# Kernel tuning notes

Hardware: AMD Instinct MI355X
Metric: run time of the kernel (lower is better)

## Reference

```python
import jax, jax.numpy as jnp
import numpy as np

N_NODES = 100000
N_EDGES = 1600000
IN_CH = 64
OUT_CH = 64


def setup_inputs() -> dict:
    key = jax.random.key(0)
    k1, k2, k3, k4, k5, k6 = jax.random.split(key, 6)
    x = jax.random.normal(k1, (N_NODES, IN_CH), dtype=jnp.float32)
    edge_index = jax.random.randint(k2, (2, N_EDGES), 0, N_NODES, dtype=jnp.int64)
    edge_attr = jax.random.uniform(k3, (N_EDGES, 3), dtype=jnp.float32)
    root_weight = jax.random.normal(k4, (IN_CH, OUT_CH), dtype=jnp.float32)
    bias = jax.random.normal(k5, (OUT_CH,), dtype=jnp.float32)
    gaussian_param = jnp.ones((1,), dtype=jnp.float32)
    return {"x": x, "edge_index": edge_index, "edge_attr": edge_attr,
            "root_weight": root_weight, "bias": bias,
            "gaussian_param": gaussian_param}


def reference(x, edge_index, edge_attr, root_weight, bias, gaussian_param):
    src = edge_index[0]
    tgt = edge_index[1]
    # per-edge gaussian weight from distance (edge_attr[:, 0])
    dist = edge_attr[:, 0:1]                                  # [E, 1]
    gw = jnp.exp(-dist ** 2 / (gaussian_param ** 2 + 1e-8))   # [E, 1]
    # gather -> matmul -> scale
    messages = (x[src] @ root_weight) * gw                    # [E, out]
    # scatter-add to target nodes
    out = jax.ops.segment_sum(messages, tgt, num_segments=x.shape[0])
    out = out + x @ root_weight + bias
    return out
```

## Files before the change

kernel.cpp:

```cpp
#include <hip/hip_runtime.h>
#include <hip/hip_bf16.h>
#include <stdint.h>

#define N_NODES 100000
#define N_EDGES 1600000
#define CH 64

#define NPB 128
#define NBUCK ((N_NODES + NPB - 1) / NPB)
#define CHUNK 4096
#define BT 1024
#define EPT (CHUNK / BT)
#define NBLK_E ((N_EDGES + CHUNK - 1) / CHUNK)

#define STRIDE 2560
#define CAP 3072
#define ST 512

#define GM 64

typedef float f32x4 __attribute__((ext_vector_type(4)));

__device__ __forceinline__ unsigned short bf16rn(float f) {
  unsigned u = __float_as_uint(f);
  unsigned r = u + 0x7FFFu + ((u >> 16) & 1u);
  return (unsigned short)(r >> 16);
}


__global__ __launch_bounds__(BT) void bin2_kernel(const int* __restrict__ ei,
                                                  const float* __restrict__ attr,
                                                  const float* __restrict__ gp,
                                                  int* __restrict__ gcur,
                                                  uint2* __restrict__ recs,
                                                  const float* __restrict__ x,
                                                  unsigned short* __restrict__ xh) {
  __shared__ int lhist[NBUCK];
  __shared__ int lbase[NBUCK];
  const int tid = threadIdx.x;
  for (int i = tid; i < NBUCK; i += BT) lhist[i] = 0;
  __syncthreads();
  const int cbase = blockIdx.x * CHUNK;
  const float inv = 1.0f / (gp[0] * gp[0] + 1e-8f);

  int s[EPT], t[EPT], lrank[EPT];
  float g[EPT];
#pragma unroll
  for (int k = 0; k < EPT; ++k) {
    const int e = cbase + k * BT + tid;
    if (e < N_EDGES) {
      s[k] = ei[e];
      t[k] = ei[N_EDGES + e];
      const float d = attr[3 * e];
      g[k] = __expf(-d * d * inv);
      lrank[k] = atomicAdd(&lhist[t[k] >> 7], 1);
    }
  }
  {
    const int nq = N_NODES * CH / 4;
    const int stride = gridDim.x * BT;
    for (int q = blockIdx.x * BT + tid; q < nq; q += stride) {
      const float4 v = reinterpret_cast<const float4*>(x)[q];
      ushort4 o;
      o.x = bf16rn(v.x);
      o.y = bf16rn(v.y);
      o.z = bf16rn(v.z);
      o.w = bf16rn(v.w);
      reinterpret_cast<ushort4*>(xh)[q] = o;
    }
  }
  __syncthreads();
  for (int i = tid; i < NBUCK; i += BT) {
    const int c = lhist[i];
    if (c) lbase[i] = i * STRIDE + atomicAdd(&gcur[i], c);
  }
  __syncthreads();

#pragma unroll
  for (int k = 0; k < EPT; ++k) {
    const int e = cbase + k * BT + tid;
    if (e < N_EDGES) {
      const int bb = t[k] >> 7;
      const int idx = lbase[bb] + lrank[k];
      if (idx < (bb + 1) * STRIDE) {
        uint2 rec;
        rec.x = (unsigned)s[k] | ((unsigned)(t[k] & (NPB - 1)) << 17);
        rec.y = __float_as_uint(g[k]);
        recs[idx] = rec;
      }
    }
  }
}

__global__ __launch_bounds__(ST) void sortb2_kernel(const int* __restrict__ gcur,
                                                    uint2* __restrict__ recs,
                                                    int* __restrict__ offs,
                                                    int* __restrict__ ends) {
  __shared__ uint2 srec[STRIDE];
  __shared__ int lhist[NPB];
  __shared__ int lofs[NPB];
  __shared__ int lcur[NPB];
  const int b = blockIdx.x;
  const int tid = threadIdx.x;
  const int start = b * STRIDE;
  int cnt = gcur[b];
  cnt = cnt < STRIDE ? cnt : STRIDE;

  if (tid < NPB) lhist[tid] = 0;
  __syncthreads();
  for (int i = tid; i < cnt; i += ST) {
    const uint2 r = recs[start + i];
    srec[i] = r;
    atomicAdd(&lhist[r.x >> 17], 1);
  }
  __syncthreads();
  if (tid < NPB) lofs[tid] = lhist[tid];
  __syncthreads();
  for (int off = 1; off < NPB; off <<= 1) {
    int t = 0;
    if (tid < NPB && tid >= off) t = lofs[tid - off];
    __syncthreads();
    if (tid < NPB) lofs[tid] += t;
    __syncthreads();
  }
  if (tid < NPB) {
    const int incl = lofs[tid];
    const int excl = incl - lhist[tid];
    lcur[tid] = excl;
    const int node = b * NPB + tid;
    if (node < N_NODES) {
      offs[node] = start + excl;
      ends[node] = start + incl;
    }
  }
  __syncthreads();
  for (int i = tid; i < cnt; i += ST) {
    const uint2 r = srec[i];
    const int pos = atomicAdd(&lcur[r.x >> 17], 1);
    recs[start + pos] = r;
  }
}


__global__ __launch_bounds__(BT) void hist2_kernel(const int* __restrict__ ei,
                                                   int* __restrict__ ghist,
                                                   const float* __restrict__ x,
                                                   unsigned short* __restrict__ xh,
                                                   int do_conv) {
  __shared__ int lh[NBUCK];
  const int tid = threadIdx.x;
  for (int i = tid; i < NBUCK; i += BT) lh[i] = 0;
  __syncthreads();
  const int cbase = blockIdx.x * CHUNK;
#pragma unroll
  for (int k = 0; k < EPT; ++k) {
    const int e = cbase + k * BT + tid;
    if (e < N_EDGES) atomicAdd(&lh[ei[N_EDGES + e] >> 7], 1);
  }
  if (do_conv) {
    const int nq = N_NODES * CH / 4;
    const int stride = gridDim.x * BT;
    for (int q = blockIdx.x * BT + tid; q < nq; q += stride) {
      const float4 v = reinterpret_cast<const float4*>(x)[q];
      ushort4 o;
      o.x = bf16rn(v.x);
      o.y = bf16rn(v.y);
      o.z = bf16rn(v.z);
      o.w = bf16rn(v.w);
      reinterpret_cast<ushort4*>(xh)[q] = o;
    }
  }
  __syncthreads();
  for (int i = tid; i < NBUCK; i += BT) {
    const int c = lh[i];
    if (c) atomicAdd(&ghist[i], c);
  }
}

__global__ __launch_bounds__(1024) void scan_kernel(const int* __restrict__ ghist,
                                                    int* __restrict__ gbase,
                                                    int* __restrict__ gcur) {
  __shared__ int sd[1024];
  const int tid = threadIdx.x;
  const int v = (tid < NBUCK) ? ghist[tid] : 0;
  sd[tid] = v;
  __syncthreads();
  for (int off = 1; off < 1024; off <<= 1) {
    int t = (tid >= off) ? sd[tid - off] : 0;
    __syncthreads();
    sd[tid] += t;
    __syncthreads();
  }
  if (tid < NBUCK) {
    const int excl = sd[tid] - v;
    gbase[tid] = excl;
    gcur[tid] = excl;
  }
}

__global__ __launch_bounds__(BT) void bin_kernel(const int* __restrict__ ei,
                                                 const float* __restrict__ attr,
                                                 const float* __restrict__ gp,
                                                 int* __restrict__ gcur,
                                                 uint2* __restrict__ recs) {
  __shared__ int lhist[NBUCK];
  __shared__ int lbase[NBUCK];
  const int tid = threadIdx.x;
  for (int i = tid; i < NBUCK; i += BT) lhist[i] = 0;
  __syncthreads();
  const int cbase = blockIdx.x * CHUNK;
  const float inv = 1.0f / (gp[0] * gp[0] + 1e-8f);

  int s[EPT], t[EPT], lrank[EPT];
  float g[EPT];
#pragma unroll
  for (int k = 0; k < EPT; ++k) {
    const int e = cbase + k * BT + tid;
    if (e < N_EDGES) {
      s[k] = ei[e];
      t[k] = ei[N_EDGES + e];
      const float d = attr[3 * e];
      g[k] = __expf(-d * d * inv);
      lrank[k] = atomicAdd(&lhist[t[k] >> 7], 1);
    }
  }
  __syncthreads();
  for (int i = tid; i < NBUCK; i += BT) {
    const int c = lhist[i];
    if (c) lbase[i] = atomicAdd(&gcur[i], c);
  }
  __syncthreads();

#pragma unroll
  for (int k = 0; k < EPT; ++k) {
    const int e = cbase + k * BT + tid;
    if (e < N_EDGES) {
      uint2 rec;
      rec.x = (unsigned)s[k] | ((unsigned)(t[k] & (NPB - 1)) << 17);
      rec.y = __float_as_uint(g[k]);
      recs[lbase[t[k] >> 7] + lrank[k]] = rec;
    }
  }
}

__global__ __launch_bounds__(ST) void sortb_kernel(const int* __restrict__ gbase,
                                                   const int* __restrict__ ghist,
                                                   uint2* __restrict__ recs,
                                                   int* __restrict__ offs) {
  __shared__ uint2 srec[CAP];
  __shared__ int lhist[NPB];
  __shared__ int lofs[NPB];
  __shared__ int lcur[NPB];
  const int b = blockIdx.x;
  const int tid = threadIdx.x;
  const int start = gbase[b];
  const int cnt = ghist[b] < CAP ? ghist[b] : CAP;

  if (tid < NPB) lhist[tid] = 0;
  __syncthreads();
  for (int i = tid; i < cnt; i += ST) {
    const uint2 r = recs[start + i];
    srec[i] = r;
    atomicAdd(&lhist[r.x >> 17], 1);
  }
  __syncthreads();
  if (tid < NPB) lofs[tid] = lhist[tid];
  __syncthreads();
  for (int off = 1; off < NPB; off <<= 1) {
    int t = 0;
    if (tid < NPB && tid >= off) t = lofs[tid - off];
    __syncthreads();
    if (tid < NPB) lofs[tid] += t;
    __syncthreads();
  }
  if (tid < NPB) {
    const int excl = lofs[tid] - lhist[tid];
    lcur[tid] = excl;
    const int node = b * NPB + tid;
    if (node < N_NODES) offs[node] = start + excl;
  }
  if (b == NBUCK - 1 && tid == 0) offs[N_NODES] = start + cnt;
  __syncthreads();
  for (int i = tid; i < cnt; i += ST) {
    const uint2 r = srec[i];
    const int pos = atomicAdd(&lcur[r.x >> 17], 1);
    recs[start + pos] = r;
  }
}


__global__ __launch_bounds__(256) void reduce7h_kernel(
    const unsigned short* __restrict__ xh, const int* __restrict__ offs,
    const int* __restrict__ ends, const uint2* __restrict__ recs,
    float* __restrict__ out) {
  const int node = (blockIdx.x * blockDim.x + threadIdx.x) >> 6;
  if (node >= N_NODES) return;
  const int lane = threadIdx.x & 63;
  const int c2 = lane & 31;
  const int eh = lane >> 5;
  const int n0 = __builtin_amdgcn_readfirstlane(offs[node]);
  const int n1 = __builtin_amdgcn_readfirstlane(ends[node]);
  const int m = n1 - n0;

  float ax = 0.0f, ay = 0.0f;
  int j = 0;
  for (; j + 16 <= m; j += 16) {
#pragma unroll
    for (int p = 0; p < 8; ++p) {
      const uint2 r0 = recs[n0 + j + 2 * p];
      const uint2 r1 = recs[n0 + j + 2 * p + 1];
      const unsigned sx = (eh ? r1.x : r0.x) & 0x1FFFFu;
      const float g = __uint_as_float(eh ? r1.y : r0.y);
      const unsigned u =
          *reinterpret_cast<const unsigned*>(&xh[(size_t)sx * CH + c2 * 2]);
      ax += g * __uint_as_float(u << 16);
      ay += g * __uint_as_float(u & 0xFFFF0000u);
    }
  }
  for (; j + 8 <= m; j += 8) {
#pragma unroll
    for (int p = 0; p < 4; ++p) {
      const uint2 r0 = recs[n0 + j + 2 * p];
      const uint2 r1 = recs[n0 + j + 2 * p + 1];
      const unsigned sx = (eh ? r1.x : r0.x) & 0x1FFFFu;
      const float g = __uint_as_float(eh ? r1.y : r0.y);
      const unsigned u =
          *reinterpret_cast<const unsigned*>(&xh[(size_t)sx * CH + c2 * 2]);
      ax += g * __uint_as_float(u << 16);
      ay += g * __uint_as_float(u & 0xFFFF0000u);
    }
  }
  for (; j < m; j += 2) {
    const uint2 r0 = recs[n0 + j];
    uint2 r1 = {0u, 0u};
    if (j + 1 < m) r1 = recs[n0 + j + 1];
    const unsigned sx = (eh ? r1.x : r0.x) & 0x1FFFFu;
    const float g = __uint_as_float(eh ? r1.y : r0.y);
    const unsigned u =
        *reinterpret_cast<const unsigned*>(&xh[(size_t)sx * CH + c2 * 2]);
    ax += g * __uint_as_float(u << 16);
    ay += g * __uint_as_float(u & 0xFFFF0000u);
  }
  ax += __shfl_xor(ax, 32);
  ay += __shfl_xor(ay, 32);
  if (lane < 32) {
    float2 o;
    o.x = ax;
    o.y = ay;
    reinterpret_cast<float2*>(out + (size_t)node * CH)[c2] = o;
  }
}

__global__ __launch_bounds__(256) void reduce3_kernel(
    const float* __restrict__ x, const int* __restrict__ offs,
    const uint2* __restrict__ recs, float* __restrict__ out) {
  const int node = (blockIdx.x * blockDim.x + threadIdx.x) >> 6;
  if (node >= N_NODES) return;
  const int lane = threadIdx.x & 63;
  const int n0 = offs[node];
  const int m = offs[node + 1] - n0;

  float acc = 0.0f;
  for (int base = 0; base < m; base += 64) {
    const int mm = (m - base) < 64 ? (m - base) : 64;
    uint2 pr = {0u, 0u};
    if (lane < mm) pr = recs[n0 + base + lane];
    const int pk_all = (int)pr.x;
    const float g_all = __uint_as_float(pr.y);
    int j = 0;
    for (; j + 4 <= mm; j += 4) {
      const int s0 = __shfl(pk_all, j + 0) & 0x1FFFF;
      const int s1 = __shfl(pk_all, j + 1) & 0x1FFFF;
      const int s2 = __shfl(pk_all, j + 2) & 0x1FFFF;
      const int s3 = __shfl(pk_all, j + 3) & 0x1FFFF;
      const float g0 = __shfl(g_all, j + 0);
      const float g1 = __shfl(g_all, j + 1);
      const float g2 = __shfl(g_all, j + 2);
      const float g3 = __shfl(g_all, j + 3);
      acc += g0 * x[(size_t)s0 * CH + lane] + g1 * x[(size_t)s1 * CH + lane] +
             g2 * x[(size_t)s2 * CH + lane] + g3 * x[(size_t)s3 * CH + lane];
    }
    for (; j < mm; ++j) {
      const int sj = __shfl(pk_all, j) & 0x1FFFF;
      const float gj = __shfl(g_all, j);
      acc += gj * x[(size_t)sj * CH + lane];
    }
  }
  out[(size_t)node * CH + lane] = acc + x[(size_t)node * CH + lane];
}

__global__ __launch_bounds__(256) void scatter_kernel(
    const float* __restrict__ x, const int* __restrict__ ei,
    const float* __restrict__ attr, const float* __restrict__ gp,
    float* __restrict__ agg) {
  const int lane = threadIdx.x & 63;
  const int wave = (blockIdx.x * blockDim.x + threadIdx.x) >> 6;
  const int nwaves = (gridDim.x * blockDim.x) >> 6;
  const float inv = 1.0f / (gp[0] * gp[0] + 1e-8f);
  for (int base = wave * 64; base < N_EDGES; base += nwaves * 64) {
    const int e = base + lane;
    const int s = ei[e];
    const int t = ei[N_EDGES + e];
    const float d = attr[3 * e];
    const float g = __expf(-d * d * inv);
#pragma unroll 1
    for (int j = 0; j < 64; ++j) {
      const int sj = __shfl(s, j);
      const int tj = __shfl(t, j);
      const float gj = __shfl(g, j);
      atomicAdd(&agg[(size_t)tj * CH + lane], gj * x[sj * CH + lane]);
    }
  }
}

__global__ __launch_bounds__(256) void rowgemm4_kernel(
    const float* __restrict__ x, const float* __restrict__ W,
    const float* __restrict__ bias, float* __restrict__ out) {
  __shared__ float sT[64][GM + 4];
  __shared__ float wl[64 * 64];
  const int tid = threadIdx.x;
  const int node0 = blockIdx.x * GM;

  {
    const float4* W4 = reinterpret_cast<const float4*>(W);
    float4* wl4 = reinterpret_cast<float4*>(wl);
#pragma unroll
    for (int i = 0; i < 4; ++i) wl4[i * 256 + tid] = W4[i * 256 + tid];
  }
  {
    const int m = tid >> 2;
    const int kq = tid & 3;
    if (node0 + m < N_NODES) {
      const float4* r4 =
          reinterpret_cast<const float4*>(out + (size_t)(node0 + m) * CH);
      const float4* x4 =
          reinterpret_cast<const float4*>(x + (size_t)(node0 + m) * CH);
#pragma unroll
      for (int q = 0; q < 4; ++q) {
        const float4 v = r4[kq * 4 + q];
        const float4 xv = x4[kq * 4 + q];
        const int k = kq * 16 + q * 4;
        sT[k + 0][m] = v.x + xv.x;
        sT[k + 1][m] = v.y + xv.y;
        sT[k + 2][m] = v.z + xv.z;
        sT[k + 3][m] = v.w + xv.w;
      }
    }
  }
  __syncthreads();

  const int m0 = (tid >> 4) * 4;
  const int c0 = (tid & 15) * 4;

  const f32x4 b4 = *reinterpret_cast<const f32x4*>(&bias[c0]);
  f32x4 acc0 = b4, acc1 = b4, acc2 = b4, acc3 = b4;

#pragma unroll 8
  for (int k = 0; k < 64; ++k) {
    const f32x4 sv = *reinterpret_cast<const f32x4*>(&sT[k][m0]);
    const f32x4 wv = *reinterpret_cast<const f32x4*>(&wl[k * 64 + c0]);
    acc0 += sv.x * wv;
    acc1 += sv.y * wv;
    acc2 += sv.z * wv;
    acc3 += sv.w * wv;
  }

  __syncthreads();
  f32x4 accs[4] = {acc0, acc1, acc2, acc3};
#pragma unroll
  for (int i = 0; i < 4; ++i) {
    const int node = node0 + m0 + i;
    if (node < N_NODES)
      *reinterpret_cast<f32x4*>(&out[(size_t)node * CH + c0]) = accs[i];
  }
}

__global__ __launch_bounds__(256) void rowgemm3_kernel(
    const float* __restrict__ W, const float* __restrict__ bias,
    float* __restrict__ out) {
  __shared__ float sT[64][GM + 4];
  __shared__ float wl[64 * 64];
  const int tid = threadIdx.x;
  const int node0 = blockIdx.x * GM;

  {
    const float4* W4 = reinterpret_cast<const float4*>(W);
    float4* wl4 = reinterpret_cast<float4*>(wl);
#pragma unroll
    for (int i = 0; i < 4; ++i) wl4[i * 256 + tid] = W4[i * 256 + tid];
  }
  {
    const int m = tid >> 2;
    const int kq = tid & 3;
    if (node0 + m < N_NODES) {
      const float4* r4 =
          reinterpret_cast<const float4*>(out + (size_t)(node0 + m) * CH);
#pragma unroll
      for (int q = 0; q < 4; ++q) {
        const float4 v = r4[kq * 4 + q];
        const int k = kq * 16 + q * 4;
        sT[k + 0][m] = v.x;
        sT[k + 1][m] = v.y;
        sT[k + 2][m] = v.z;
        sT[k + 3][m] = v.w;
      }
    }
  }
  __syncthreads();

  const int m0 = (tid >> 4) * 4;
  const int c0 = (tid & 15) * 4;

  const f32x4 b4 = *reinterpret_cast<const f32x4*>(&bias[c0]);
  f32x4 acc0 = b4, acc1 = b4, acc2 = b4, acc3 = b4;

#pragma unroll 8
  for (int k = 0; k < 64; ++k) {
    const f32x4 sv = *reinterpret_cast<const f32x4*>(&sT[k][m0]);
    const f32x4 wv = *reinterpret_cast<const f32x4*>(&wl[k * 64 + c0]);
    acc0 += sv.x * wv;
    acc1 += sv.y * wv;
    acc2 += sv.z * wv;
    acc3 += sv.w * wv;
  }

  __syncthreads();
  f32x4 accs[4] = {acc0, acc1, acc2, acc3};
#pragma unroll
  for (int i = 0; i < 4; ++i) {
    const int node = node0 + m0 + i;
    if (node < N_NODES)
      *reinterpret_cast<f32x4*>(&out[(size_t)node * CH + c0]) = accs[i];
  }
}

__global__ __launch_bounds__(256) void rowgemm_kernel(
    const float* __restrict__ x, const float* __restrict__ W,
    const float* __restrict__ bias, float* __restrict__ out) {
  const int r = blockIdx.x * blockDim.x + threadIdx.x;
  if (r >= N_NODES) return;
  const float* xr = x + (size_t)r * CH;
  float* outr = out + (size_t)r * CH;

  float s[CH];
#pragma unroll
  for (int k4 = 0; k4 < CH / 4; ++k4) {
    float4 xv = *reinterpret_cast<const float4*>(xr + k4 * 4);
    float4 av = *reinterpret_cast<const float4*>(outr + k4 * 4);
    s[k4 * 4 + 0] = xv.x + av.x;
    s[k4 * 4 + 1] = xv.y + av.y;
    s[k4 * 4 + 2] = xv.z + av.z;
    s[k4 * 4 + 3] = xv.w + av.w;
  }

  float acc[CH];
#pragma unroll
  for (int c = 0; c < CH; ++c) acc[c] = bias[c];

#pragma unroll
  for (int k = 0; k < CH; ++k) {
    const float sk = s[k];
#pragma unroll
    for (int c4 = 0; c4 < CH / 4; ++c4) {
      const float4 w = *reinterpret_cast<const float4*>(&W[k * CH + c4 * 4]);
      acc[c4 * 4 + 0] += sk * w.x;
      acc[c4 * 4 + 1] += sk * w.y;
      acc[c4 * 4 + 2] += sk * w.z;
      acc[c4 * 4 + 3] += sk * w.w;
    }
  }

#pragma unroll
  for (int c4 = 0; c4 < CH / 4; ++c4) {
    float4 o = {acc[c4 * 4 + 0], acc[c4 * 4 + 1], acc[c4 * 4 + 2],
                acc[c4 * 4 + 3]};
    *reinterpret_cast<float4*>(outr + c4 * 4) = o;
  }
}

extern "C" void kernel_launch(void* const* d_in, const int* in_sizes, int n_in,
                              void* d_out, int out_size, void* d_ws,
                              size_t ws_size, hipStream_t stream) {
  const float* x = (const float*)d_in[0];
  const int* ei = (const int*)d_in[1];
  const float* attr = (const float*)d_in[2];
  const float* W = (const float*)d_in[3];
  const float* bias = (const float*)d_in[4];
  const float* gp = (const float*)d_in[5];
  float* out = (float*)d_out;

  const size_t sz_i = ((size_t)NBUCK * 4 + 255) & ~(size_t)255;
  const size_t sz_xh = (size_t)N_NODES * CH * 2;
  const size_t sz_offs1 = ((size_t)N_NODES * 4 + 255) & ~(size_t)255;

  const size_t sz_recsA = (size_t)NBUCK * STRIDE * 8;
  const size_t need_fs = sz_i + sz_recsA + 2 * sz_offs1 + sz_xh;

  const size_t sz_recsB = (size_t)N_EDGES * 8;
  const size_t sz_offsB = ((size_t)(N_NODES + 1) * 4 + 255) & ~(size_t)255;
  const size_t need_b = 3 * sz_i + sz_recsB + sz_offsB;
  const size_t need_a = need_b + sz_xh;

  if (ws_size >= need_fs) {
    char* base = (char*)d_ws;
    int* gcur = (int*)base;
    uint2* recs = (uint2*)(base + sz_i);
    int* offs = (int*)(base + sz_i + sz_recsA);
    int* ends = (int*)(base + sz_i + sz_recsA + sz_offs1);
    unsigned short* xh =
        (unsigned short*)(base + sz_i + sz_recsA + 2 * sz_offs1);

    hipMemsetAsync(gcur, 0, (size_t)NBUCK * 4, stream);
    bin2_kernel<<<NBLK_E, BT, 0, stream>>>(ei, attr, gp, gcur, recs, x, xh);
    sortb2_kernel<<<NBUCK, ST, 0, stream>>>(gcur, recs, offs, ends);
    reduce7h_kernel<<<(N_NODES * 64 + 255) / 256, 256, 0, stream>>>(
        xh, offs, ends, recs, out);
    rowgemm4_kernel<<<(N_NODES + GM - 1) / GM, 256, 0, stream>>>(x, W, bias,
                                                                 out);
  } else if (ws_size >= need_b) {
    char* base = (char*)d_ws;
    int* ghist = (int*)base;
    int* gbase = (int*)(base + sz_i);
    int* gcur = (int*)(base + 2 * sz_i);
    uint2* recs = (uint2*)(base + 3 * sz_i);
    int* offs = (int*)(base + 3 * sz_i + sz_recsB);
    unsigned short* xh = (unsigned short*)(base + need_b);

    const int tier_a = (ws_size >= need_a) ? 1 : 0;
    hipMemsetAsync(ghist, 0, (size_t)NBUCK * 4, stream);
    hist2_kernel<<<NBLK_E, BT, 0, stream>>>(ei, ghist, x, xh, tier_a);
    scan_kernel<<<1, 1024, 0, stream>>>(ghist, gbase, gcur);
    bin_kernel<<<NBLK_E, BT, 0, stream>>>(ei, attr, gp, gcur, recs);
    sortb_kernel<<<NBUCK, ST, 0, stream>>>(gbase, ghist, recs, offs);
    if (tier_a) {
      reduce7h_kernel<<<(N_NODES * 64 + 255) / 256, 256, 0, stream>>>(
          xh, offs, offs + 1, recs, out);
      rowgemm4_kernel<<<(N_NODES + GM - 1) / GM, 256, 0, stream>>>(x, W, bias,
                                                                   out);
    } else {
      reduce3_kernel<<<(N_NODES * 64 + 255) / 256, 256, 0, stream>>>(x, offs,
                                                                     recs, out);
      rowgemm3_kernel<<<(N_NODES + GM - 1) / GM, 256, 0, stream>>>(W, bias,
                                                                   out);
    }
  } else {
    hipMemsetAsync(out, 0, (size_t)N_NODES * CH * sizeof(float), stream);
    scatter_kernel<<<2048, 256, 0, stream>>>(x, ei, attr, gp, out);
    rowgemm_kernel<<<(N_NODES + 255) / 256, 256, 0, stream>>>(x, W, bias, out);
  }
}
```

Measured before the change: 105.7 us.

## Store edge aggregate as bf16 scratch and fuse add into row GEMM

A new reduce kernel writes the per-node gathered-x aggregate as packed bf16 to a workspace buffer instead of fp32 into the output. A new row-GEMM kernel reads that aggregate, adds x, and does a single matmul with bias, so the output is written once rather than written and then read back. The sort kernel's block size also grows from 512 to 1024 threads. This cuts HBM traffic for the aggregate, but rounding the sum to bf16 adds precision loss and the path needs extra workspace.

```diff
diff --git a/kernel.cpp b/kernel.cpp
--- a/kernel.cpp
+++ b/kernel.cpp
@@ -15,7 +15,7 @@
 
 #define STRIDE 2560
 #define CAP 3072
-#define ST 512
+#define ST 1024
 
 #define GM 64
 
@@ -25,6 +25,10 @@
   unsigned u = __float_as_uint(f);
   unsigned r = u + 0x7FFFu + ((u >> 16) & 1u);
   return (unsigned short)(r >> 16);
+}
+
+__device__ __forceinline__ float bf16f(unsigned short h) {
+  return __uint_as_float((unsigned)h << 16);
 }
 
 
@@ -288,6 +292,67 @@
   }
 }
 
+
+__global__ __launch_bounds__(256) void reduce7hb_kernel(
+    const unsigned short* __restrict__ xh, const int* __restrict__ offs,
+    const int* __restrict__ ends, const uint2* __restrict__ recs,
+    unsigned* __restrict__ aggh) {
+  const int node = (blockIdx.x * blockDim.x + threadIdx.x) >> 6;
+  if (node >= N_NODES) return;
+  const int lane = threadIdx.x & 63;
+  const int c2 = lane & 31;
+  const int eh = lane >> 5;
+  const int n0 = __builtin_amdgcn_readfirstlane(offs[node]);
+  const int n1 = __builtin_amdgcn_readfirstlane(ends[node]);
+  const int m = n1 - n0;
+
+  float ax = 0.0f, ay = 0.0f;
+  int j = 0;
+  for (; j + 16 <= m; j += 16) {
+#pragma unroll
+    for (int p = 0; p < 8; ++p) {
+      const uint2 r0 = recs[n0 + j + 2 * p];
+      const uint2 r1 = recs[n0 + j + 2 * p + 1];
+      const unsigned sx = (eh ? r1.x : r0.x) & 0x1FFFFu;
+      const float g = __uint_as_float(eh ? r1.y : r0.y);
+      const unsigned u =
+          *reinterpret_cast<const unsigned*>(&xh[(size_t)sx * CH + c2 * 2]);
+      ax += g * __uint_as_float(u << 16);
+      ay += g * __uint_as_float(u & 0xFFFF0000u);
+    }
+  }
+  for (; j + 8 <= m; j += 8) {
+#pragma unroll
+    for (int p = 0; p < 4; ++p) {
+      const uint2 r0 = recs[n0 + j + 2 * p];
+      const uint2 r1 = recs[n0 + j + 2 * p + 1];
+      const unsigned sx = (eh ? r1.x : r0.x) & 0x1FFFFu;
+      const float g = __uint_as_float(eh ? r1.y : r0.y);
+      const unsigned u =
+          *reinterpret_cast<const unsigned*>(&xh[(size_t)sx * CH + c2 * 2]);
+      ax += g * __uint_as_float(u << 16);
+      ay += g * __uint_as_float(u & 0xFFFF0000u);
+    }
+  }
+  for (; j < m; j += 2) {
+    const uint2 r0 = recs[n0 + j];
+    uint2 r1 = {0u, 0u};
+    if (j + 1 < m) r1 = recs[n0 + j + 1];
+    const unsigned sx = (eh ? r1.x : r0.x) & 0x1FFFFu;
+    const float g = __uint_as_float(eh ? r1.y : r0.y);
+    const unsigned u =
+        *reinterpret_cast<const unsigned*>(&xh[(size_t)sx * CH + c2 * 2]);
+    ax += g * __uint_as_float(u << 16);
+    ay += g * __uint_as_float(u & 0xFFFF0000u);
+  }
+  ax += __shfl_xor(ax, 32);
+  ay += __shfl_xor(ay, 32);
+  if (lane < 32) {
+    const unsigned pk =
+        ((unsigned)bf16rn(ay) << 16) | (unsigned)bf16rn(ax);
+    aggh[(size_t)node * 32 + c2] = pk;
+  }
+}
 
 __global__ __launch_bounds__(256) void reduce7h_kernel(
     const unsigned short* __restrict__ xh, const int* __restrict__ offs,
@@ -413,6 +478,69 @@
   }
 }
 
+__global__ __launch_bounds__(256) void rowgemm5_kernel(
+    const unsigned short* __restrict__ aggh, const float* __restrict__ x,
+    const float* __restrict__ W, const float* __restrict__ bias,
+    float* __restrict__ out) {
+  __shared__ float sT[64][GM + 4];
+  __shared__ float wl[64 * 64];
+  const int tid = threadIdx.x;
+  const int node0 = blockIdx.x * GM;
+
+  {
+    const float4* W4 = reinterpret_cast<const float4*>(W);
+    float4* wl4 = reinterpret_cast<float4*>(wl);
+#pragma unroll
+    for (int i = 0; i < 4; ++i) wl4[i * 256 + tid] = W4[i * 256 + tid];
+  }
+  {
+    const int m = tid >> 2;
+    const int kq = tid & 3;
+    if (node0 + m < N_NODES) {
+      const float4* x4 =
+          reinterpret_cast<const float4*>(x + (size_t)(node0 + m) * CH);
+      const uint2* a2 = reinterpret_cast<const uint2*>(
+          aggh + (size_t)(node0 + m) * CH + kq * 16);
+#pragma unroll
+      for (int q = 0; q < 4; ++q) {
+        const uint2 hv = a2[q];
+        const float4 xv = x4[kq * 4 + q];
+        const int k = kq * 16 + q * 4;
+        sT[k + 0][m] = bf16f((unsigned short)(hv.x & 0xFFFF)) + xv.x;
+        sT[k + 1][m] = bf16f((unsigned short)(hv.x >> 16)) + xv.y;
+        sT[k + 2][m] = bf16f((unsigned short)(hv.y & 0xFFFF)) + xv.z;
+        sT[k + 3][m] = bf16f((unsigned short)(hv.y >> 16)) + xv.w;
+      }
+    }
+  }
+  __syncthreads();
+
+  const int m0 = (tid >> 4) * 4;
+  const int c0 = (tid & 15) * 4;
+
+  const f32x4 b4 = *reinterpret_cast<const f32x4*>(&bias[c0]);
+  f32x4 acc0 = b4, acc1 = b4, acc2 = b4, acc3 = b4;
+
+#pragma unroll 8
+  for (int k = 0; k < 64; ++k) {
+    const f32x4 sv = *reinterpret_cast<const f32x4*>(&sT[k][m0]);
+    const f32x4 wv = *reinterpret_cast<const f32x4*>(&wl[k * 64 + c0]);
+    acc0 += sv.x * wv;
+    acc1 += sv.y * wv;
+    acc2 += sv.z * wv;
+    acc3 += sv.w * wv;
+  }
+
+  __syncthreads();
+  f32x4 accs[4] = {acc0, acc1, acc2, acc3};
+#pragma unroll
+  for (int i = 0; i < 4; ++i) {
+    const int node = node0 + m0 + i;
+    if (node < N_NODES)
+      *reinterpret_cast<f32x4*>(&out[(size_t)node * CH + c0]) = accs[i];
+  }
+}
+
 __global__ __launch_bounds__(256) void rowgemm4_kernel(
     const float* __restrict__ x, const float* __restrict__ W,
     const float* __restrict__ bias, float* __restrict__ out) {
@@ -592,9 +720,11 @@
   const size_t sz_i = ((size_t)NBUCK * 4 + 255) & ~(size_t)255;
   const size_t sz_xh = (size_t)N_NODES * CH * 2;
   const size_t sz_offs1 = ((size_t)N_NODES * 4 + 255) & ~(size_t)255;
+  const size_t sz_aggh = ((size_t)N_NODES * CH * 2 + 255) & ~(size_t)255;
 
   const size_t sz_recsA = (size_t)NBUCK * STRIDE * 8;
   const size_t need_fs = sz_i + sz_recsA + 2 * sz_offs1 + sz_xh;
+  const size_t need_fs2 = need_fs + sz_aggh;
 
   const size_t sz_recsB = (size_t)N_EDGES * 8;
   const size_t sz_offsB = ((size_t)(N_NODES + 1) * 4 + 255) & ~(size_t)255;
@@ -609,14 +739,22 @@
     int* ends = (int*)(base + sz_i + sz_recsA + sz_offs1);
     unsigned short* xh =
         (unsigned short*)(base + sz_i + sz_recsA + 2 * sz_offs1);
+    unsigned short* aggh = (unsigned short*)(base + need_fs);
 
     hipMemsetAsync(gcur, 0, (size_t)NBUCK * 4, stream);
     bin2_kernel<<<NBLK_E, BT, 0, stream>>>(ei, attr, gp, gcur, recs, x, xh);
     sortb2_kernel<<<NBUCK, ST, 0, stream>>>(gcur, recs, offs, ends);
-    reduce7h_kernel<<<(N_NODES * 64 + 255) / 256, 256, 0, stream>>>(
-        xh, offs, ends, recs, out);
-    rowgemm4_kernel<<<(N_NODES + GM - 1) / GM, 256, 0, stream>>>(x, W, bias,
-                                                                 out);
+    if (ws_size >= need_fs2) {
+      reduce7hb_kernel<<<(N_NODES * 64 + 255) / 256, 256, 0, stream>>>(
+          xh, offs, ends, recs, (unsigned*)aggh);
+      rowgemm5_kernel<<<(N_NODES + GM - 1) / GM, 256, 0, stream>>>(
+          aggh, x, W, bias, out);
+    } else {
+      reduce7h_kernel<<<(N_NODES * 64 + 255) / 256, 256, 0, stream>>>(
+          xh, offs, ends, recs, out);
+      rowgemm4_kernel<<<(N_NODES + GM - 1) / GM, 256, 0, stream>>>(x, W, bias,
+                                                                   out);
+    }
   } else if (ws_size >= need_b) {
     char* base = (char*)d_ws;
     int* ghist = (int*)base;
```

Result: no change. 104.4 us (-1.2%).
